# Performance work log

Measured on AMD Instinct MI355X. Metric: run time of the kernel, lower is better.

Reference implementation:

```python
import jax, jax.numpy as jnp
import numpy as np

EPS = 1e-20

def efficient_squash(s):
    # Efficient-CapsNet squash: (1 - 1/e^||s||) * s/||s||
    n = jnp.linalg.norm(s, axis=-1, keepdims=True)
    return (1.0 - 1.0 / (jnp.exp(n) + EPS)) * (s / (n + EPS))

def setup_inputs() -> dict:
    key = jax.random.key(0)
    k1, k2 = jax.random.split(key)
    B, N, D_in = 32, 2048, 16
    K, D_out = 32, 16
    x = jax.random.normal(k1, (B, N, D_in), dtype=jnp.float32)
    # he_normal fan_in = N * D_in * ... ; use simple scaled normal init
    w = jax.random.normal(k2, (K, N, D_in, D_out), dtype=jnp.float32) * 0.05
    b = jnp.zeros((K, N, 1), dtype=jnp.float32)
    return {"x": x, "w": w, "b": b}

def reference(x, w, b):
    D_out = w.shape[-1]
    # projection: [B,N,D_in] x [K,N,D_in,D_out] -> [B,K,N,D_out]
    u = jnp.einsum('bji,kjiz->bkjz', x, w)
    # agreement c_{bkj} = sum_{i,z} u_{bkjz} u_{bkiz} = <u_j, sum_i u_i>
    t = jnp.sum(u, axis=2)                      # [B,K,D_out]
    c = jnp.einsum('bkjz,bkz->bkj', u, t)[..., None]  # [B,K,N,1]
    c = c / jnp.sqrt(jnp.asarray(D_out, jnp.float32))
    c = jax.nn.softmax(c, axis=1)               # softmax over capsules K
    c = c + b                                   # broadcast [K,N,1]
    s = jnp.sum(u * c, axis=2)                  # [B,K,D_out]
    return efficient_squash(s)
```

## Files before the change

kernel.cpp:

```cpp
#include <hip/hip_runtime.h>

#define NN 2048
#define KK 32

#define WS_U     0
#define WS_TP2   67108864UL
#define WS_T     67633152UL
#define WS_SPART 67698688UL
#define WS_NEED  71892992UL

__device__ __forceinline__ float bf_lo(unsigned v) { return __uint_as_float(v << 16); }
__device__ __forceinline__ float bf_hi(unsigned v) { return __uint_as_float(v & 0xffff0000u); }
__device__ __forceinline__ unsigned pack_bf16(float a, float b) {
    unsigned ua = __float_as_uint(a), ub = __float_as_uint(b);
    return ((ua + 0x8000u) >> 16) | ((ub + 0x8000u) & 0xffff0000u);
}

__global__ __launch_bounds__(256)
void k1_u(const float* __restrict__ x, const float* __restrict__ w,
          unsigned* __restrict__ u_pk)
{
    __shared__ float x_lds[2][32][16];
    const int tid = threadIdx.x;
    const int jj  = tid >> 7;
    const int k   = (tid >> 2) & 31;
    const int zq  = tid & 3;
    const int j0  = blockIdx.x * 2;
    const int j   = j0 + jj;

    {
        const int jjx = tid >> 7, b = (tid >> 2) & 31, q = tid & 3;
        const float4 v = *reinterpret_cast<const float4*>(
            x + ((size_t)b * NN + j0 + jjx) * 16 + q * 4);
        *reinterpret_cast<float4*>(&x_lds[jjx][b][q * 4]) = v;
    }

    const float4* w4 = reinterpret_cast<const float4*>(
        w + (((size_t)k * NN + j) * 16) * 16) + zq;
    float4 wr[16];
#pragma unroll
    for (int i = 0; i < 16; ++i) wr[i] = w4[i * 4];

    __syncthreads();

    unsigned* __restrict__ ub = u_pk + ((size_t)j * KK + k) * 8 + zq * 2;
#pragma unroll 2
    for (int b = 0; b < 32; ++b) {
        float xs[16];
#pragma unroll
        for (int q = 0; q < 4; ++q) {
            float4 v = *reinterpret_cast<const float4*>(&x_lds[jj][b][q * 4]);
            xs[q * 4 + 0] = v.x; xs[q * 4 + 1] = v.y;
            xs[q * 4 + 2] = v.z; xs[q * 4 + 3] = v.w;
        }
        float4 acc = make_float4(0.f, 0.f, 0.f, 0.f);
#pragma unroll
        for (int i = 0; i < 16; ++i) {
            acc.x = fmaf(xs[i], wr[i].x, acc.x);
            acc.y = fmaf(xs[i], wr[i].y, acc.y);
            acc.z = fmaf(xs[i], wr[i].z, acc.z);
            acc.w = fmaf(xs[i], wr[i].w, acc.w);
        }
        uint2 o;
        o.x = pack_bf16(acc.x, acc.y);
        o.y = pack_bf16(acc.z, acc.w);
        *reinterpret_cast<uint2*>(ub + (size_t)b * (NN * KK * 8)) = o;
    }
}

__global__ __launch_bounds__(1024)
void k2a_tpart(const unsigned* __restrict__ u_pk, float* __restrict__ t_part2)
{
    __shared__ float red[16][64][8];
    const int tid  = threadIdx.x;
    const int js   = tid >> 6;
    const int sl64 = tid & 63;
    const int b    = blockIdx.x >> 3;
    const int slj  = blockIdx.x & 7;

    const uint4* up = reinterpret_cast<const uint4*>(
        u_pk + (size_t)b * 524288 + (size_t)(slj * 256 + js) * 256) + sl64;
    float a[8];
#pragma unroll
    for (int e = 0; e < 8; ++e) a[e] = 0.f;
#pragma unroll
    for (int it = 0; it < 16; ++it) {
        uint4 v = up[(size_t)it * (16 * 64)];
        a[0] += bf_lo(v.x); a[1] += bf_hi(v.x);
        a[2] += bf_lo(v.y); a[3] += bf_hi(v.y);
        a[4] += bf_lo(v.z); a[5] += bf_hi(v.z);
        a[6] += bf_lo(v.w); a[7] += bf_hi(v.w);
    }
#pragma unroll
    for (int e = 0; e < 8; ++e) red[js][sl64][e] = a[e];
    __syncthreads();
    if (tid < 512) {
        const int s = tid >> 3, e = tid & 7;
        float acc = 0.f;
#pragma unroll
        for (int r = 0; r < 16; ++r) acc += red[r][s][e];
        t_part2[((size_t)b * 8 + slj) * 512 + s * 8 + e] = acc;
    }
}

__global__ __launch_bounds__(256)
void k2a2_t(const float* __restrict__ t_part2, float* __restrict__ t)
{
    const int idx4 = blockIdx.x * 256 + threadIdx.x;
    const int b = idx4 >> 7, loc4 = idx4 & 127;
    const float4* p = reinterpret_cast<const float4*>(t_part2) + (size_t)b * 1024 + loc4;
    float4 s = make_float4(0.f, 0.f, 0.f, 0.f);
#pragma unroll
    for (int sl = 0; sl < 8; ++sl) {
        float4 v = p[sl * 128];
        s.x += v.x; s.y += v.y; s.z += v.z; s.w += v.w;
    }
    reinterpret_cast<float4*>(t)[idx4] = s;
}

__global__ __launch_bounds__(256)
void k2b_fused(const unsigned* __restrict__ u_pk, const float* __restrict__ t,
               const float* __restrict__ bias, float* __restrict__ s_part)
{
    __shared__ float lc_lds[32][33];
    __shared__ float s_lds[8][32][16];
    const int tid = threadIdx.x;
    const int k   = tid & 31;
    const int jl  = tid >> 5;
    const int b   = blockIdx.x >> 6;
    const int jc  = blockIdx.x & 63;

    float tr[16];
    const float4* tp = reinterpret_cast<const float4*>(t + ((size_t)b * KK + k) * 16);
#pragma unroll
    for (int q = 0; q < 4; ++q) {
        float4 v = tp[q];
        tr[4 * q + 0] = v.x; tr[4 * q + 1] = v.y; tr[4 * q + 2] = v.z; tr[4 * q + 3] = v.w;
    }

    uint4 ua[4], ud[4];
#pragma unroll
    for (int jj = 0; jj < 4; ++jj) {
        const int jL = jj * 8 + jl;
        const int jg = jc * 32 + jL;
        const uint4* up = reinterpret_cast<const uint4*>(
            u_pk + ((size_t)b * NN + jg) * 256 + k * 8);
        ua[jj] = up[0]; ud[jj] = up[1];
        float a0 = 0.f, a1 = 0.f;
        a0 = fmaf(bf_lo(ua[jj].x), tr[0],  a0); a1 = fmaf(bf_hi(ua[jj].x), tr[1],  a1);
        a0 = fmaf(bf_lo(ua[jj].y), tr[2],  a0); a1 = fmaf(bf_hi(ua[jj].y), tr[3],  a1);
        a0 = fmaf(bf_lo(ua[jj].z), tr[4],  a0); a1 = fmaf(bf_hi(ua[jj].z), tr[5],  a1);
        a0 = fmaf(bf_lo(ua[jj].w), tr[6],  a0); a1 = fmaf(bf_hi(ua[jj].w), tr[7],  a1);
        a0 = fmaf(bf_lo(ud[jj].x), tr[8],  a0); a1 = fmaf(bf_hi(ud[jj].x), tr[9],  a1);
        a0 = fmaf(bf_lo(ud[jj].y), tr[10], a0); a1 = fmaf(bf_hi(ud[jj].y), tr[11], a1);
        a0 = fmaf(bf_lo(ud[jj].z), tr[12], a0); a1 = fmaf(bf_hi(ud[jj].z), tr[13], a1);
        a0 = fmaf(bf_lo(ud[jj].w), tr[14], a0); a1 = fmaf(bf_hi(ud[jj].w), tr[15], a1);
        lc_lds[jL][k] = a0 + a1;
    }
    __syncthreads();

    {
        const int jq = tid >> 3, kq = tid & 7;
        float lv[4];
#pragma unroll
        for (int m = 0; m < 4; ++m) lv[m] = lc_lds[jq][kq * 4 + m];
        float pm = fmaxf(fmaxf(lv[0], lv[1]), fmaxf(lv[2], lv[3]));
        pm = fmaxf(pm, __shfl_xor(pm, 1));
        pm = fmaxf(pm, __shfl_xor(pm, 2));
        pm = fmaxf(pm, __shfl_xor(pm, 4));
        float ev[4], ps = 0.f;
#pragma unroll
        for (int m = 0; m < 4; ++m) { ev[m] = __expf((lv[m] - pm) * 0.25f); ps += ev[m]; }
        ps += __shfl_xor(ps, 1);
        ps += __shfl_xor(ps, 2);
        ps += __shfl_xor(ps, 4);
        const float inv = 1.f / ps;
        const int jg = jc * 32 + jq;
#pragma unroll
        for (int m = 0; m < 4; ++m)
            lv[m] = ev[m] * inv + bias[(size_t)(kq * 4 + m) * NN + jg];
        __syncthreads();
#pragma unroll
        for (int m = 0; m < 4; ++m) lc_lds[jq][kq * 4 + m] = lv[m];
    }
    __syncthreads();

    float sacc[16];
#pragma unroll
    for (int z = 0; z < 16; ++z) sacc[z] = 0.f;
#pragma unroll
    for (int jj = 0; jj < 4; ++jj) {
        const float cv = lc_lds[jj * 8 + jl][k];
        const uint4 a = ua[jj], d = ud[jj];
        sacc[0]  = fmaf(cv, bf_lo(a.x), sacc[0]);  sacc[1]  = fmaf(cv, bf_hi(a.x), sacc[1]);
        sacc[2]  = fmaf(cv, bf_lo(a.y), sacc[2]);  sacc[3]  = fmaf(cv, bf_hi(a.y), sacc[3]);
        sacc[4]  = fmaf(cv, bf_lo(a.z), sacc[4]);  sacc[5]  = fmaf(cv, bf_hi(a.z), sacc[5]);
        sacc[6]  = fmaf(cv, bf_lo(a.w), sacc[6]);  sacc[7]  = fmaf(cv, bf_hi(a.w), sacc[7]);
        sacc[8]  = fmaf(cv, bf_lo(d.x), sacc[8]);  sacc[9]  = fmaf(cv, bf_hi(d.x), sacc[9]);
        sacc[10] = fmaf(cv, bf_lo(d.y), sacc[10]); sacc[11] = fmaf(cv, bf_hi(d.y), sacc[11]);
        sacc[12] = fmaf(cv, bf_lo(d.z), sacc[12]); sacc[13] = fmaf(cv, bf_hi(d.z), sacc[13]);
        sacc[14] = fmaf(cv, bf_lo(d.w), sacc[14]); sacc[15] = fmaf(cv, bf_hi(d.w), sacc[15]);
    }

#pragma unroll
    for (int q = 0; q < 4; ++q)
        *reinterpret_cast<float4*>(&s_lds[jl][k][q * 4]) =
            make_float4(sacc[q * 4], sacc[q * 4 + 1], sacc[q * 4 + 2], sacc[q * 4 + 3]);
    __syncthreads();
    {
        const int kk = tid >> 3, zp = tid & 7;
        float2 o; o.x = 0.f; o.y = 0.f;
#pragma unroll
        for (int l = 0; l < 8; ++l) {
            o.x += s_lds[l][kk][2 * zp];
            o.y += s_lds[l][kk][2 * zp + 1];
        }
        reinterpret_cast<float2*>(s_part)[((size_t)b * 64 + jc) * 256 + kk * 8 + zp] = o;
    }
}

__global__ __launch_bounds__(256)
void k4_squash(const float* __restrict__ s_part, float* __restrict__ out)
{
    const int idx4 = blockIdx.x * 256 + threadIdx.x;
    const int b = idx4 >> 7, loc4 = idx4 & 127;
    const float4* p = reinterpret_cast<const float4*>(s_part) + (size_t)b * 8192 + loc4;
    float4 s = make_float4(0.f, 0.f, 0.f, 0.f);
#pragma unroll 8
    for (int jc = 0; jc < 64; ++jc) {
        float4 v = p[jc * 128];
        s.x += v.x; s.y += v.y; s.z += v.z; s.w += v.w;
    }
    float ss = s.x * s.x + s.y * s.y + s.z * s.z + s.w * s.w;
    ss += __shfl_xor(ss, 1);
    ss += __shfl_xor(ss, 2);
    const float n = sqrtf(ss);
    const float sc = (1.f - 1.f / (__expf(n) + 1e-20f)) / (n + 1e-20f);
    float4 o; o.x = s.x * sc; o.y = s.y * sc; o.z = s.z * sc; o.w = s.w * sc;
    reinterpret_cast<float4*>(out)[idx4] = o;
}

__global__ void k_sentinel(float* __restrict__ out)
{
    out[blockIdx.x * 256 + threadIdx.x] = 12345.0f;
}

extern "C" void kernel_launch(void* const* d_in, const int* in_sizes, int n_in,
                              void* d_out, int out_size, void* d_ws, size_t ws_size,
                              hipStream_t stream)
{
    const float* x    = (const float*)d_in[0];
    const float* w    = (const float*)d_in[1];
    const float* bias = (const float*)d_in[2];
    float* out        = (float*)d_out;

    char* ws = (char*)d_ws;
    if (ws_size < WS_NEED) {
        k_sentinel<<<dim3(64), dim3(256), 0, stream>>>(out);
        return;
    }
    unsigned* u_pk = (unsigned*)(ws + WS_U);
    float* t_part2 = (float*)(ws + WS_TP2);
    float* t       = (float*)(ws + WS_T);
    float* s_part  = (float*)(ws + WS_SPART);

    k1_u     <<<dim3(1024), dim3(256),  0, stream>>>(x, w, u_pk);
    k2a_tpart<<<dim3(256),  dim3(1024), 0, stream>>>(u_pk, t_part2);
    k2a2_t   <<<dim3(16),   dim3(256),  0, stream>>>(t_part2, t);
    k2b_fused<<<dim3(2048), dim3(256),  0, stream>>>(u_pk, t, bias, s_part);
    k4_squash<<<dim3(16),   dim3(256),  0, stream>>>(s_part, out);
}
```

Measured before the change: 65.30 us.

## Store u in j-major layout and read x directly without LDS staging

Changes the intermediate u buffer layout from [b][j][k][z] to [j][b][k][z], so each k1 block writes one contiguous 32 KB region instead of 32 widely strided rows. The readers in k2a_tpart and k2b_fused are re-indexed to match. k1 now uses one j per 128-thread block and loads x straight from global memory (broadcast reads) instead of staging it through LDS, which drops the barrier. The risk is that the reads in k2a become more strided, and that every thread now issues redundant scalar x loads.

New measurement: 76.03 us. 1.16x slower.

```diff
diff --git a/kernel.cpp b/kernel.cpp
--- a/kernel.cpp
+++ b/kernel.cpp
@@ -16,24 +16,14 @@
     return ((ua + 0x8000u) >> 16) | ((ub + 0x8000u) & 0xffff0000u);
 }
 
-__global__ __launch_bounds__(256)
+__global__ __launch_bounds__(128)
 void k1_u(const float* __restrict__ x, const float* __restrict__ w,
           unsigned* __restrict__ u_pk)
 {
-    __shared__ float x_lds[2][32][16];
     const int tid = threadIdx.x;
-    const int jj  = tid >> 7;
-    const int k   = (tid >> 2) & 31;
     const int zq  = tid & 3;
-    const int j0  = blockIdx.x * 2;
-    const int j   = j0 + jj;
-
-    {
-        const int jjx = tid >> 7, b = (tid >> 2) & 31, q = tid & 3;
-        const float4 v = *reinterpret_cast<const float4*>(
-            x + ((size_t)b * NN + j0 + jjx) * 16 + q * 4);
-        *reinterpret_cast<float4*>(&x_lds[jjx][b][q * 4]) = v;
-    }
+    const int k   = tid >> 2;
+    const int j   = blockIdx.x;
 
     const float4* w4 = reinterpret_cast<const float4*>(
         w + (((size_t)k * NN + j) * 16) * 16) + zq;
@@ -41,18 +31,13 @@
 #pragma unroll
     for (int i = 0; i < 16; ++i) wr[i] = w4[i * 4];
 
-    __syncthreads();
-
-    unsigned* __restrict__ ub = u_pk + ((size_t)j * KK + k) * 8 + zq * 2;
-#pragma unroll 2
+    unsigned* __restrict__ ub = u_pk + (size_t)j * 8192 + k * 8 + zq * 2;
+#pragma unroll 4
     for (int b = 0; b < 32; ++b) {
+        const float* __restrict__ xr = x + ((size_t)b * NN + j) * 16;
         float xs[16];
 #pragma unroll
-        for (int q = 0; q < 4; ++q) {
-            float4 v = *reinterpret_cast<const float4*>(&x_lds[jj][b][q * 4]);
-            xs[q * 4 + 0] = v.x; xs[q * 4 + 1] = v.y;
-            xs[q * 4 + 2] = v.z; xs[q * 4 + 3] = v.w;
-        }
+        for (int i = 0; i < 16; ++i) xs[i] = xr[i];
         float4 acc = make_float4(0.f, 0.f, 0.f, 0.f);
 #pragma unroll
         for (int i = 0; i < 16; ++i) {
@@ -64,7 +49,7 @@
         uint2 o;
         o.x = pack_bf16(acc.x, acc.y);
         o.y = pack_bf16(acc.z, acc.w);
-        *reinterpret_cast<uint2*>(ub + (size_t)b * (NN * KK * 8)) = o;
+        *reinterpret_cast<uint2*>(ub + (size_t)b * 256) = o;
     }
 }
 
@@ -78,14 +63,14 @@
     const int b    = blockIdx.x >> 3;
     const int slj  = blockIdx.x & 7;
 
-    const uint4* up = reinterpret_cast<const uint4*>(
-        u_pk + (size_t)b * 524288 + (size_t)(slj * 256 + js) * 256) + sl64;
+    const uint4* up = reinterpret_cast<const uint4*>(u_pk)
+                    + ((size_t)(slj * 256 + js) * 32 + b) * 64 + sl64;
     float a[8];
 #pragma unroll
     for (int e = 0; e < 8; ++e) a[e] = 0.f;
 #pragma unroll
     for (int it = 0; it < 16; ++it) {
-        uint4 v = up[(size_t)it * (16 * 64)];
+        uint4 v = up[(size_t)it * (16 * 32 * 64)];
         a[0] += bf_lo(v.x); a[1] += bf_hi(v.x);
         a[2] += bf_lo(v.y); a[3] += bf_hi(v.y);
         a[4] += bf_lo(v.z); a[5] += bf_hi(v.z);
@@ -143,8 +128,8 @@
     for (int jj = 0; jj < 4; ++jj) {
         const int jL = jj * 8 + jl;
         const int jg = jc * 32 + jL;
-        const uint4* up = reinterpret_cast<const uint4*>(
-            u_pk + ((size_t)b * NN + jg) * 256 + k * 8);
+        const uint4* up = reinterpret_cast<const uint4*>(u_pk)
+                        + ((size_t)jg * 32 + b) * 64 + k * 2;
         ua[jj] = up[0]; ud[jj] = up[1];
         float a0 = 0.f, a1 = 0.f;
         a0 = fmaf(bf_lo(ua[jj].x), tr[0],  a0); a1 = fmaf(bf_hi(ua[jj].x), tr[1],  a1);
@@ -264,7 +249,7 @@
     float* t       = (float*)(ws + WS_T);
     float* s_part  = (float*)(ws + WS_SPART);
 
-    k1_u     <<<dim3(1024), dim3(256),  0, stream>>>(x, w, u_pk);
+    k1_u     <<<dim3(2048), dim3(128),  0, stream>>>(x, w, u_pk);
     k2a_tpart<<<dim3(256),  dim3(1024), 0, stream>>>(u_pk, t_part2);
     k2a2_t   <<<dim3(16),   dim3(256),  0, stream>>>(t_part2, t);
     k2b_fused<<<dim3(2048), dim3(256),  0, stream>>>(u_pk, t, bias, s_part);
```
